# Performance work log

Measured on AMD Instinct MI355X. Metric: run time of the kernel, lower is better.

The kernel has to match this reference:

```python
import jax, jax.numpy as jnp
import numpy as np

SESSION_CHANNELS = [128, 160, 192, 224, 240, 248, 252, 256]  # per-session channel counts
N_SESS = len(SESSION_CHANNELS)
B, MAX_C, MAX_T = 16, 256, 4096
HID, N_SRC = 512, 256


def setup_inputs() -> dict:
    key = jax.random.key(0)
    ks = jax.random.split(key, 7)
    session_ids = jax.random.randint(ks[0], (B,), 0, N_SESS)
    chan_table = jnp.asarray(SESSION_CHANNELS)
    channel_counts = chan_table[session_ids]
    seq_lens = jax.random.randint(ks[1], (B,), MAX_T // 2, MAX_T + 1)
    x = jax.random.normal(ks[2], (B, MAX_C, MAX_T), jnp.float32)
    # zero-pad beyond true channels and true time (as the docstring states)
    cmask = (jnp.arange(MAX_C)[None, :] < channel_counts[:, None]).astype(x.dtype)
    tmask = (jnp.arange(MAX_T)[None, :] < seq_lens[:, None]).astype(x.dtype)
    x = x * cmask[:, :, None] * tmask[:, None, :]
    # per-session Linear(num_channels -> HID), padded to MAX_C rows (torch-style uniform init)
    lim1 = 1.0 / np.sqrt(MAX_C)
    W_sess = jax.random.uniform(ks[3], (N_SESS, MAX_C, HID), jnp.float32, -lim1, lim1)
    b_sess = jax.random.uniform(ks[4], (N_SESS, HID), jnp.float32, -lim1, lim1)
    lim2 = 1.0 / np.sqrt(HID)
    W2 = jax.random.uniform(ks[5], (HID, N_SRC), jnp.float32, -lim2, lim2)
    b2 = jax.random.uniform(ks[6], (N_SRC,), jnp.float32, -lim2, lim2)
    return dict(x=x, session_ids=session_ids, channel_counts=channel_counts,
                seq_lens=seq_lens, W_sess=W_sess, b_sess=b_sess, W2=W2, b2=b2)


def reference(x, session_ids, channel_counts, seq_lens, W_sess, b_sess, W2, b2):
    # mask padded channels so the full-width contraction equals the sliced per-sample matmul
    cmask = (jnp.arange(x.shape[1])[None, :] < channel_counts[:, None]).astype(x.dtype)
    xm = x * cmask[:, :, None]                       # (B, Max_C, Max_T)
    W = W_sess[session_ids]                          # (B, Max_C, HID) gathered per sample
    b = b_sess[session_ids]                          # (B, HID)
    h = jnp.einsum('bct,bch->bht', xm, W) + b[:, :, None]
    h = jax.nn.gelu(h, approximate=False)            # torch nn.GELU default is exact erf
    out = jnp.einsum('bht,hs->bst', h, W2) + b2[None, :, None]  # (B, N_SRC, Max_T)
    tmask = (jnp.arange(x.shape[2])[None, :] < seq_lens[:, None]).astype(x.dtype)
    return out * tmask[:, None, :]
```

## Files before the change

### kernel.cpp

```cpp
#include <hip/hip_runtime.h>

typedef __attribute__((ext_vector_type(8))) _Float16 f16x8;
typedef __attribute__((ext_vector_type(4))) _Float16 f16x4;
typedef __attribute__((ext_vector_type(4))) float f32x4;

#define NB 16
#define MAXC 256
#define MAXT 4096
#define HID 512
#define NSRC 256
#define TT 64

__device__ __forceinline__ float gelu_fast(float x) {
  float p = x * x;
  float q = __builtin_fmaf(p, -0.10294336f, -2.30220778f);
  float e = __builtin_amdgcn_exp2f(x * q);
  return x * __builtin_amdgcn_rcpf(1.0f + e);
}

__global__ void transpose_cvt_kernel(const float* __restrict__ src,
                                     _Float16* __restrict__ dst, int R, int C) {
  __shared__ float tile[32][33];
  const float* s = src + (size_t)blockIdx.z * R * C;
  _Float16* d = dst + (size_t)blockIdx.z * R * C;
  int c0 = blockIdx.x * 32, r0 = blockIdx.y * 32;
  int tx = threadIdx.x, ty = threadIdx.y;
  for (int i = ty; i < 32; i += 8)
    tile[i][tx] = s[(size_t)(r0 + i) * C + (c0 + tx)];
  __syncthreads();
  for (int i = ty; i < 32; i += 8)
    d[(size_t)(c0 + i) * R + (r0 + tx)] = (_Float16)tile[tx][i];
}

__global__ __launch_bounds__(512, 4)
void fused_sess_proj_kernel(const float* __restrict__ x,
                            const int* __restrict__ sess_ids,
                            const int* __restrict__ seq_lens,
                            const _Float16* __restrict__ W1t,
                            const float* __restrict__ b_sess,
                            const _Float16* __restrict__ W2t,
                            const float* __restrict__ b2,
                            float* __restrict__ out) {
  int wg = blockIdx.x;
  int b = wg >> 6;
  int t0 = (wg & 63) * TT;
  int seqlen = seq_lens[b];
  int tid = threadIdx.x;

  if (t0 >= seqlen) {
    int row = tid >> 1;
    int part = tid & 1;
    float* po = out + ((size_t)b * NSRC + row) * MAXT + t0 + part * 32;
    f32x4 z = {0.f, 0.f, 0.f, 0.f};
    #pragma unroll
    for (int i = 0; i < 8; ++i) *(f32x4*)(po + i * 4) = z;
    return;
  }

  __shared__ _Float16 Xs[TT * MAXC];
  __shared__ _Float16 Hs[TT * 256];

  {
    int c = tid & 255;
    int th = tid >> 8;
    const float* xp = x + ((size_t)b * MAXC + c) * MAXT + t0 + th * 32;
    #pragma unroll
    for (int i = 0; i < 8; ++i) {
      f32x4 v = *(const f32x4*)(xp + i * 4);
      #pragma unroll
      for (int k = 0; k < 4; ++k) {
        int t = th * 32 + i * 4 + k;
        Xs[t * 256 + (c ^ ((t & 7) << 3))] = (_Float16)v[k];
      }
    }
  }
  __syncthreads();

  int lane = tid & 63;
  int w = tid >> 6;
  int lg = lane >> 4;
  int lr = lane & 15;
  int sid = sess_ids[b];
  const _Float16* W1s = W1t + (size_t)sid * HID * MAXC;

  f32x4 acc2[2][4];
  #pragma unroll
  for (int mi = 0; mi < 2; ++mi) {
    f32x4 bv = *(const f32x4*)(b2 + w * 32 + mi * 16 + lg * 4);
    #pragma unroll
    for (int ni = 0; ni < 4; ++ni) acc2[mi][ni] = bv;
  }

  #pragma unroll
  for (int ch = 0; ch < 2; ++ch) {
    f32x4 acc1[2][4];
    #pragma unroll
    for (int mi = 0; mi < 2; ++mi) {
      f32x4 bv = *(const f32x4*)(b_sess + sid * HID + ch * 256 + w * 32 + mi * 16 + lg * 4);
      #pragma unroll
      for (int ni = 0; ni < 4; ++ni) acc1[mi][ni] = bv;
    }
    #pragma unroll
    for (int ks = 0; ks < 8; ++ks) {
      int k0 = ks * 32;
      f16x8 af[2], bf[4];
      #pragma unroll
      for (int mi = 0; mi < 2; ++mi)
        af[mi] = *(const f16x8*)(W1s +
            (size_t)(ch * 256 + w * 32 + mi * 16 + lr) * MAXC + k0 + lg * 8);
      #pragma unroll
      for (int ni = 0; ni < 4; ++ni) {
        int t = ni * 16 + lr;
        bf[ni] = *(const f16x8*)(&Xs[t * 256 + ((k0 + lg * 8) ^ ((t & 7) << 3))]);
      }
      #pragma unroll
      for (int mi = 0; mi < 2; ++mi)
        #pragma unroll
        for (int ni = 0; ni < 4; ++ni)
          acc1[mi][ni] = __builtin_amdgcn_mfma_f32_16x16x32_f16(af[mi], bf[ni], acc1[mi][ni], 0, 0, 0);
    }
    #pragma unroll
    for (int mi = 0; mi < 2; ++mi) {
      int hh = w * 32 + mi * 16 + lg * 4;
      #pragma unroll
      for (int ni = 0; ni < 4; ++ni) {
        int t = ni * 16 + lr;
        f16x4 g;
        #pragma unroll
        for (int r = 0; r < 4; ++r) g[r] = (_Float16)gelu_fast(acc1[mi][ni][r]);
        *(f16x4*)(&Hs[t * 256 + (hh ^ ((t & 7) << 3))]) = g;
      }
    }
    __syncthreads();
    #pragma unroll
    for (int ks = 0; ks < 8; ++ks) {
      int k0 = ks * 32;
      f16x8 af[2], bf[4];
      #pragma unroll
      for (int mi = 0; mi < 2; ++mi)
        af[mi] = *(const f16x8*)(W2t +
            (size_t)(w * 32 + mi * 16 + lr) * HID + ch * 256 + k0 + lg * 8);
      #pragma unroll
      for (int ni = 0; ni < 4; ++ni) {
        int t = ni * 16 + lr;
        bf[ni] = *(const f16x8*)(&Hs[t * 256 + ((k0 + lg * 8) ^ ((t & 7) << 3))]);
      }
      #pragma unroll
      for (int mi = 0; mi < 2; ++mi)
        #pragma unroll
        for (int ni = 0; ni < 4; ++ni)
          acc2[mi][ni] = __builtin_amdgcn_mfma_f32_16x16x32_f16(af[mi], bf[ni], acc2[mi][ni], 0, 0, 0);
    }
    __syncthreads();
  }

  #pragma unroll
  for (int mi = 0; mi < 2; ++mi) {
    int s0 = w * 32 + mi * 16 + lg * 4;
    #pragma unroll
    for (int ni = 0; ni < 4; ++ni) {
      int t = t0 + ni * 16 + lr;
      float m = (t < seqlen) ? 1.0f : 0.0f;
      #pragma unroll
      for (int r = 0; r < 4; ++r)
        out[((size_t)b * NSRC + s0 + r) * MAXT + t] = acc2[mi][ni][r] * m;
    }
  }
}

extern "C" void kernel_launch(void* const* d_in, const int* in_sizes, int n_in,
                              void* d_out, int out_size, void* d_ws, size_t ws_size,
                              hipStream_t stream) {
  const float* x      = (const float*)d_in[0];
  const int* sess     = (const int*)d_in[1];
  const int* seq      = (const int*)d_in[3];
  const float* W_sess = (const float*)d_in[4];
  const float* b_sess = (const float*)d_in[5];
  const float* W2     = (const float*)d_in[6];
  const float* b2     = (const float*)d_in[7];
  float* out = (float*)d_out;

  _Float16* W1t = (_Float16*)d_ws;
  _Float16* W2t = (_Float16*)((char*)d_ws + (size_t)8 * HID * MAXC * sizeof(_Float16));

  dim3 tb(32, 8);
  transpose_cvt_kernel<<<dim3(HID / 32, MAXC / 32, 8), tb, 0, stream>>>(W_sess, W1t, MAXC, HID);
  transpose_cvt_kernel<<<dim3(NSRC / 32, HID / 32, 1), tb, 0, stream>>>(W2, W2t, HID, NSRC);

  fused_sess_proj_kernel<<<dim3(NB * (MAXT / TT)), dim3(512), 0, stream>>>(
      x, sess, seq, W1t, b_sess, W2t, b2, out);
}
```

Before: 90.30 us.

## Retile fused MLP to 32-token blocks with 32x32x16 MFMA and 4 waves

Halves the time tile to 32 tokens and uses 256-thread blocks with 32x32x16 MFMA instructions, giving each wave a 64-row slice of the output. The X load now packs two channels per convert and store, the swizzle widens to 32 rows, and the barriers switch to a lighter lgkmcnt-only form, with the trailing barrier on the last chunk removed. MFMA issue is wrapped in setprio. The smaller tile doubles the block count and cuts LDS per block, which should raise occupancy and skip padded tokens more finely, at the cost of reading the weights from global memory twice as often per token.

```diff
diff --git a/kernel.cpp b/kernel.cpp
--- a/kernel.cpp
+++ b/kernel.cpp
@@ -2,14 +2,24 @@
 
 typedef __attribute__((ext_vector_type(8))) _Float16 f16x8;
 typedef __attribute__((ext_vector_type(4))) _Float16 f16x4;
+typedef __attribute__((ext_vector_type(2))) __fp16 fp16v2;
 typedef __attribute__((ext_vector_type(4))) float f32x4;
+typedef __attribute__((ext_vector_type(16))) float f32x16;
 
 #define NB 16
 #define MAXC 256
 #define MAXT 4096
 #define HID 512
 #define NSRC 256
-#define TT 64
+#define TT 32
+
+#define BAR() asm volatile("s_waitcnt lgkmcnt(0)\n\ts_barrier" ::: "memory")
+
+#define MFMA32(a, b, c) __builtin_amdgcn_mfma_f32_32x32x16_f16(a, b, c, 0, 0, 0)
+
+__device__ __forceinline__ int swz(int t, int col) {
+  return t * 256 + (col ^ ((t & 31) << 3));
+}
 
 __device__ __forceinline__ float gelu_fast(float x) {
   float p = x * x;
@@ -32,7 +42,7 @@
     d[(size_t)(c0 + i) * R + (r0 + tx)] = (_Float16)tile[tx][i];
 }
 
-__global__ __launch_bounds__(512, 4)
+__global__ __launch_bounds__(256, 4)
 void fused_sess_proj_kernel(const float* __restrict__ x,
                             const int* __restrict__ sess_ids,
                             const int* __restrict__ seq_lens,
@@ -42,15 +52,13 @@
                             const float* __restrict__ b2,
                             float* __restrict__ out) {
   int wg = blockIdx.x;
-  int b = wg >> 6;
-  int t0 = (wg & 63) * TT;
+  int b = wg >> 7;
+  int t0 = (wg & 127) * TT;
   int seqlen = seq_lens[b];
   int tid = threadIdx.x;
 
   if (t0 >= seqlen) {
-    int row = tid >> 1;
-    int part = tid & 1;
-    float* po = out + ((size_t)b * NSRC + row) * MAXT + t0 + part * 32;
+    float* po = out + ((size_t)b * NSRC + tid) * MAXT + t0;
     f32x4 z = {0.f, 0.f, 0.f, 0.f};
     #pragma unroll
     for (int i = 0; i < 8; ++i) *(f32x4*)(po + i * 4) = z;
@@ -60,112 +68,110 @@
   __shared__ _Float16 Xs[TT * MAXC];
   __shared__ _Float16 Hs[TT * 256];
 
+  int lane = tid & 63;
+  int w = tid >> 6;
+  int lm = lane & 31;
+  int kl = lane >> 5;
+  int sid = sess_ids[b];
+  const _Float16* W1s = W1t + (size_t)sid * HID * MAXC;
+
   {
-    int c = tid & 255;
-    int th = tid >> 8;
-    const float* xp = x + ((size_t)b * MAXC + c) * MAXT + t0 + th * 32;
+    int c2 = (tid & 127) * 2;
+    int th = tid >> 7;
+    const float* xp = x + ((size_t)b * MAXC + c2) * MAXT + t0 + th * 16;
     #pragma unroll
-    for (int i = 0; i < 8; ++i) {
-      f32x4 v = *(const f32x4*)(xp + i * 4);
+    for (int half = 0; half < 2; ++half) {
+      f32x4 va[2], vb[2];
       #pragma unroll
-      for (int k = 0; k < 4; ++k) {
-        int t = th * 32 + i * 4 + k;
-        Xs[t * 256 + (c ^ ((t & 7) << 3))] = (_Float16)v[k];
+      for (int i = 0; i < 2; ++i) va[i] = *(const f32x4*)(xp + half * 8 + i * 4);
+      #pragma unroll
+      for (int i = 0; i < 2; ++i) vb[i] = *(const f32x4*)(xp + MAXT + half * 8 + i * 4);
+      #pragma unroll
+      for (int k = 0; k < 8; ++k) {
+        int t = th * 16 + half * 8 + k;
+        fp16v2 p = __builtin_amdgcn_cvt_pkrtz(va[k >> 2][k & 3], vb[k >> 2][k & 3]);
+        *(fp16v2*)(&Xs[swz(t, c2)]) = p;
       }
     }
   }
-  __syncthreads();
+  BAR();
 
-  int lane = tid & 63;
-  int w = tid >> 6;
-  int lg = lane >> 4;
-  int lr = lane & 15;
-  int sid = sess_ids[b];
-  const _Float16* W1s = W1t + (size_t)sid * HID * MAXC;
-
-  f32x4 acc2[2][4];
-  #pragma unroll
-  for (int mi = 0; mi < 2; ++mi) {
-    f32x4 bv = *(const f32x4*)(b2 + w * 32 + mi * 16 + lg * 4);
-    #pragma unroll
-    for (int ni = 0; ni < 4; ++ni) acc2[mi][ni] = bv;
-  }
+  f32x16 acc2[2];
 
   #pragma unroll
   for (int ch = 0; ch < 2; ++ch) {
-    f32x4 acc1[2][4];
+    int chb = ch * 256;
+
+    f32x16 acc1[2];
     #pragma unroll
-    for (int mi = 0; mi < 2; ++mi) {
-      f32x4 bv = *(const f32x4*)(b_sess + sid * HID + ch * 256 + w * 32 + mi * 16 + lg * 4);
+    for (int mi = 0; mi < 2; ++mi)
       #pragma unroll
-      for (int ni = 0; ni < 4; ++ni) acc1[mi][ni] = bv;
+      for (int q = 0; q < 4; ++q) {
+        f32x4 bv = *(const f32x4*)(b_sess + sid * HID + chb + w * 64 + mi * 32 + q * 8 + kl * 4);
+        #pragma unroll
+        for (int r = 0; r < 4; ++r) acc1[mi][q * 4 + r] = bv[r];
+      }
+
+    const _Float16* w1p = W1s + (size_t)(chb + w * 64 + lm) * MAXC + kl * 8;
+    #pragma unroll
+    for (int ks = 0; ks < 16; ++ks) {
+      f16x8 af0 = *(const f16x8*)(w1p + ks * 16);
+      f16x8 af1 = *(const f16x8*)(w1p + 32 * MAXC + ks * 16);
+      f16x8 bf = *(const f16x8*)(&Xs[swz(lm, ks * 16 + kl * 8)]);
+      __builtin_amdgcn_s_setprio(1);
+      acc1[0] = MFMA32(af0, bf, acc1[0]);
+      acc1[1] = MFMA32(af1, bf, acc1[1]);
+      __builtin_amdgcn_s_setprio(0);
     }
+
     #pragma unroll
-    for (int ks = 0; ks < 8; ++ks) {
-      int k0 = ks * 32;
-      f16x8 af[2], bf[4];
+    for (int mi = 0; mi < 2; ++mi)
       #pragma unroll
-      for (int mi = 0; mi < 2; ++mi)
-        af[mi] = *(const f16x8*)(W1s +
-            (size_t)(ch * 256 + w * 32 + mi * 16 + lr) * MAXC + k0 + lg * 8);
-      #pragma unroll
-      for (int ni = 0; ni < 4; ++ni) {
-        int t = ni * 16 + lr;
-        bf[ni] = *(const f16x8*)(&Xs[t * 256 + ((k0 + lg * 8) ^ ((t & 7) << 3))]);
+      for (int q = 0; q < 4; ++q) {
+        int hh = w * 64 + mi * 32 + q * 8 + kl * 4;
+        f16x4 g;
+        #pragma unroll
+        for (int r = 0; r < 4; ++r) g[r] = (_Float16)gelu_fast(acc1[mi][q * 4 + r]);
+        *(f16x4*)(&Hs[swz(lm, hh)]) = g;
       }
+
+    if (ch == 0) {
       #pragma unroll
       for (int mi = 0; mi < 2; ++mi)
         #pragma unroll
-        for (int ni = 0; ni < 4; ++ni)
-          acc1[mi][ni] = __builtin_amdgcn_mfma_f32_16x16x32_f16(af[mi], bf[ni], acc1[mi][ni], 0, 0, 0);
+        for (int q = 0; q < 4; ++q) {
+          f32x4 bv = *(const f32x4*)(b2 + w * 64 + mi * 32 + q * 8 + kl * 4);
+          #pragma unroll
+          for (int r = 0; r < 4; ++r) acc2[mi][q * 4 + r] = bv[r];
+        }
     }
+    BAR();
+
+    const _Float16* w2p = W2t + (size_t)(w * 64 + lm) * HID + chb + kl * 8;
     #pragma unroll
-    for (int mi = 0; mi < 2; ++mi) {
-      int hh = w * 32 + mi * 16 + lg * 4;
-      #pragma unroll
-      for (int ni = 0; ni < 4; ++ni) {
-        int t = ni * 16 + lr;
-        f16x4 g;
-        #pragma unroll
-        for (int r = 0; r < 4; ++r) g[r] = (_Float16)gelu_fast(acc1[mi][ni][r]);
-        *(f16x4*)(&Hs[t * 256 + (hh ^ ((t & 7) << 3))]) = g;
-      }
+    for (int ks = 0; ks < 16; ++ks) {
+      f16x8 af0 = *(const f16x8*)(w2p + ks * 16);
+      f16x8 af1 = *(const f16x8*)(w2p + 32 * HID + ks * 16);
+      f16x8 bf = *(const f16x8*)(&Hs[swz(lm, ks * 16 + kl * 8)]);
+      __builtin_amdgcn_s_setprio(1);
+      acc2[0] = MFMA32(af0, bf, acc2[0]);
+      acc2[1] = MFMA32(af1, bf, acc2[1]);
+      __builtin_amdgcn_s_setprio(0);
     }
-    __syncthreads();
-    #pragma unroll
-    for (int ks = 0; ks < 8; ++ks) {
-      int k0 = ks * 32;
-      f16x8 af[2], bf[4];
-      #pragma unroll
-      for (int mi = 0; mi < 2; ++mi)
-        af[mi] = *(const f16x8*)(W2t +
-            (size_t)(w * 32 + mi * 16 + lr) * HID + ch * 256 + k0 + lg * 8);
-      #pragma unroll
-      for (int ni = 0; ni < 4; ++ni) {
-        int t = ni * 16 + lr;
-        bf[ni] = *(const f16x8*)(&Hs[t * 256 + ((k0 + lg * 8) ^ ((t & 7) << 3))]);
-      }
-      #pragma unroll
-      for (int mi = 0; mi < 2; ++mi)
-        #pragma unroll
-        for (int ni = 0; ni < 4; ++ni)
-          acc2[mi][ni] = __builtin_amdgcn_mfma_f32_16x16x32_f16(af[mi], bf[ni], acc2[mi][ni], 0, 0, 0);
-    }
-    __syncthreads();
+    if (ch == 0) BAR();
   }
 
+  int t = t0 + lm;
+  float m = (t < seqlen) ? 1.0f : 0.0f;
   #pragma unroll
-  for (int mi = 0; mi < 2; ++mi) {
-    int s0 = w * 32 + mi * 16 + lg * 4;
+  for (int mi = 0; mi < 2; ++mi)
     #pragma unroll
-    for (int ni = 0; ni < 4; ++ni) {
-      int t = t0 + ni * 16 + lr;
-      float m = (t < seqlen) ? 1.0f : 0.0f;
+    for (int q = 0; q < 4; ++q) {
+      int s0 = w * 64 + mi * 32 + q * 8 + kl * 4;
       #pragma unroll
       for (int r = 0; r < 4; ++r)
-        out[((size_t)b * NSRC + s0 + r) * MAXT + t] = acc2[mi][ni][r] * m;
+        out[((size_t)b * NSRC + s0 + r) * MAXT + t] = acc2[mi][q * 4 + r] * m;
     }
-  }
 }
 
 extern "C" void kernel_launch(void* const* d_in, const int* in_sizes, int n_in,
@@ -187,6 +193,6 @@
   transpose_cvt_kernel<<<dim3(HID / 32, MAXC / 32, 8), tb, 0, stream>>>(W_sess, W1t, MAXC, HID);
   transpose_cvt_kernel<<<dim3(NSRC / 32, HID / 32, 1), tb, 0, stream>>>(W2, W2t, HID, NSRC);
 
-  fused_sess_proj_kernel<<<dim3(NB * (MAXT / TT)), dim3(512), 0, stream>>>(
+  fused_sess_proj_kernel<<<dim3(NB * (MAXT / TT)), dim3(256), 0, stream>>>(
       x, sess, seq, W1t, b_sess, W2t, b2, out);
 }
```

Measured after the change: 150.3 us. 66.4% more time.

## Split fused projection into two tiled GEMM kernels with fp16 hidden buffer

Applied to the files above, without the earlier changes.

Replaces the single fused kernel, which kept the whole hidden activation in LDS per 64-step time tile, with two separate GEMM kernels using 128x128 tiles, K-chunked LDS staging and 4x4 MFMA tiles per wave. The GELU hidden activation is written to a global fp16 workspace buffer (B x T x HID) and read back by the second GEMM. The goal is higher MFMA register reuse and better occupancy, and it also adds pkrtz conversion and setprio around the MFMA blocks. The cost is an extra global round trip for the hidden tensor, about 64MB written and then read, plus one more launch.

```diff
diff --git a/kernel.cpp b/kernel.cpp
--- a/kernel.cpp
+++ b/kernel.cpp
@@ -2,6 +2,7 @@
 
 typedef __attribute__((ext_vector_type(8))) _Float16 f16x8;
 typedef __attribute__((ext_vector_type(4))) _Float16 f16x4;
+typedef __attribute__((ext_vector_type(2))) __fp16 fp16v2;
 typedef __attribute__((ext_vector_type(4))) float f32x4;
 
 #define NB 16
@@ -9,7 +10,10 @@
 #define MAXT 4096
 #define HID 512
 #define NSRC 256
-#define TT 64
+
+#define BAR() asm volatile("s_waitcnt lgkmcnt(0)\n\ts_barrier" ::: "memory")
+
+#define MFMA(a, b, c) __builtin_amdgcn_mfma_f32_16x16x32_f16(a, b, c, 0, 0, 0)
 
 __device__ __forceinline__ float gelu_fast(float x) {
   float p = x * x;
@@ -32,138 +36,198 @@
     d[(size_t)(c0 + i) * R + (r0 + tx)] = (_Float16)tile[tx][i];
 }
 
-__global__ __launch_bounds__(512, 4)
-void fused_sess_proj_kernel(const float* __restrict__ x,
-                            const int* __restrict__ sess_ids,
-                            const int* __restrict__ seq_lens,
-                            const _Float16* __restrict__ W1t,
-                            const float* __restrict__ b_sess,
-                            const _Float16* __restrict__ W2t,
-                            const float* __restrict__ b2,
-                            float* __restrict__ out) {
+
+__global__ __launch_bounds__(256, 3)
+void gemm1_kernel(const float* __restrict__ x,
+                  const int* __restrict__ sess_ids,
+                  const int* __restrict__ seq_lens,
+                  const _Float16* __restrict__ W1t,
+                  const float* __restrict__ b_sess,
+                  _Float16* __restrict__ h_t) {
   int wg = blockIdx.x;
+  int nt = wg & 31;
+  int mt = (wg >> 5) & 3;
+  int b = wg >> 7;
+  int tb0 = nt * 128, h0 = mt * 128;
+  int seqlen = seq_lens[b];
+  if (tb0 >= seqlen) return;
+  int sid = sess_ids[b];
+  const _Float16* W = W1t + (size_t)sid * HID * MAXC + (size_t)h0 * MAXC;
+
+  __shared__ _Float16 As[128 * 64];
+  __shared__ _Float16 Bs[128 * 64];
+
+  int tid = threadIdx.x;
+  int lane = tid & 63, w = tid >> 6;
+  int wr = w >> 1, wc = w & 1;
+  int lg = lane >> 4, lr = lane & 15;
+
+  f32x4 acc[4][4];
+  #pragma unroll
+  for (int mi = 0; mi < 4; ++mi) {
+    f32x4 bv = *(const f32x4*)(b_sess + sid * HID + h0 + wr * 64 + mi * 16 + lg * 4);
+    #pragma unroll
+    for (int ni = 0; ni < 4; ++ni) acc[mi][ni] = bv;
+  }
+
+  int ar = tid >> 1, ah = tid & 1;
+  int c2 = (tid & 31) * 2, ts = tid >> 5;
+
+  #pragma unroll 1
+  for (int kc = 0; kc < 4; ++kc) {
+    int c0 = kc * 64;
+    {
+      const _Float16* ga = W + (size_t)ar * MAXC + c0 + ah * 32;
+      #pragma unroll
+      for (int j = 0; j < 4; ++j) {
+        f16x8 v = *(const f16x8*)(ga + j * 8);
+        *(f16x8*)(&As[ar * 64 + (((ah * 4 + j) ^ (ar & 7)) * 8)]) = v;
+      }
+    }
+    {
+      const float* gx = x + ((size_t)b * MAXC + c0 + c2) * MAXT + tb0 + ts * 16;
+      f32x4 va[4], vb[4];
+      #pragma unroll
+      for (int j = 0; j < 4; ++j) va[j] = *(const f32x4*)(gx + j * 4);
+      #pragma unroll
+      for (int j = 0; j < 4; ++j) vb[j] = *(const f32x4*)(gx + MAXT + j * 4);
+      #pragma unroll
+      for (int k = 0; k < 16; ++k) {
+        int t = ts * 16 + k;
+        fp16v2 p = __builtin_amdgcn_cvt_pkrtz(va[k >> 2][k & 3], vb[k >> 2][k & 3]);
+        *(fp16v2*)(&Bs[t * 64 + (((c2 >> 3) ^ (t & 7)) * 8) + (c2 & 7)]) = p;
+      }
+    }
+    BAR();
+    #pragma unroll
+    for (int slot = 0; slot < 2; ++slot) {
+      f16x8 af[4], bf[4];
+      #pragma unroll
+      for (int mi = 0; mi < 4; ++mi) {
+        int row = wr * 64 + mi * 16 + lr;
+        af[mi] = *(const f16x8*)(&As[row * 64 + (((slot * 4 + lg) ^ (row & 7)) * 8)]);
+      }
+      #pragma unroll
+      for (int ni = 0; ni < 4; ++ni) {
+        int t = wc * 64 + ni * 16 + lr;
+        bf[ni] = *(const f16x8*)(&Bs[t * 64 + (((slot * 4 + lg) ^ (t & 7)) * 8)]);
+      }
+      __builtin_amdgcn_s_setprio(1);
+      #pragma unroll
+      for (int mi = 0; mi < 4; ++mi)
+        #pragma unroll
+        for (int ni = 0; ni < 4; ++ni)
+          acc[mi][ni] = MFMA(af[mi], bf[ni], acc[mi][ni]);
+      __builtin_amdgcn_s_setprio(0);
+    }
+    BAR();
+  }
+
+  _Float16* hp = h_t + (size_t)b * MAXT * HID;
+  #pragma unroll
+  for (int mi = 0; mi < 4; ++mi) {
+    int h = h0 + wr * 64 + mi * 16 + lg * 4;
+    #pragma unroll
+    for (int ni = 0; ni < 4; ++ni) {
+      int t = tb0 + wc * 64 + ni * 16 + lr;
+      f16x4 g;
+      #pragma unroll
+      for (int r = 0; r < 4; ++r) g[r] = (_Float16)gelu_fast(acc[mi][ni][r]);
+      *(f16x4*)(hp + (size_t)t * HID + h) = g;
+    }
+  }
+}
+
+__global__ __launch_bounds__(256, 4)
+void gemm2_kernel(const int* __restrict__ seq_lens,
+                  const _Float16* __restrict__ W2t,
+                  const float* __restrict__ b2,
+                  const _Float16* __restrict__ h_t,
+                  float* __restrict__ out) {
+  int wg = blockIdx.x;
+  int nt = wg & 31;
+  int mt = (wg >> 5) & 1;
   int b = wg >> 6;
-  int t0 = (wg & 63) * TT;
+  int tb0 = nt * 128, s0 = mt * 128;
   int seqlen = seq_lens[b];
   int tid = threadIdx.x;
 
-  if (t0 >= seqlen) {
-    int row = tid >> 1;
-    int part = tid & 1;
-    float* po = out + ((size_t)b * NSRC + row) * MAXT + t0 + part * 32;
+  if (tb0 >= seqlen) {
+    int sr = tid >> 1, tq = (tid & 1) * 64;
+    float* po = out + ((size_t)b * NSRC + s0 + sr) * MAXT + tb0 + tq;
     f32x4 z = {0.f, 0.f, 0.f, 0.f};
     #pragma unroll
-    for (int i = 0; i < 8; ++i) *(f32x4*)(po + i * 4) = z;
+    for (int i = 0; i < 16; ++i) *(f32x4*)(po + i * 4) = z;
     return;
   }
 
-  __shared__ _Float16 Xs[TT * MAXC];
-  __shared__ _Float16 Hs[TT * 256];
-
-  {
-    int c = tid & 255;
-    int th = tid >> 8;
-    const float* xp = x + ((size_t)b * MAXC + c) * MAXT + t0 + th * 32;
-    #pragma unroll
-    for (int i = 0; i < 8; ++i) {
-      f32x4 v = *(const f32x4*)(xp + i * 4);
-      #pragma unroll
-      for (int k = 0; k < 4; ++k) {
-        int t = th * 32 + i * 4 + k;
-        Xs[t * 256 + (c ^ ((t & 7) << 3))] = (_Float16)v[k];
-      }
-    }
-  }
-  __syncthreads();
-
-  int lane = tid & 63;
-  int w = tid >> 6;
-  int lg = lane >> 4;
-  int lr = lane & 15;
-  int sid = sess_ids[b];
-  const _Float16* W1s = W1t + (size_t)sid * HID * MAXC;
-
-  f32x4 acc2[2][4];
-  #pragma unroll
-  for (int mi = 0; mi < 2; ++mi) {
-    f32x4 bv = *(const f32x4*)(b2 + w * 32 + mi * 16 + lg * 4);
-    #pragma unroll
-    for (int ni = 0; ni < 4; ++ni) acc2[mi][ni] = bv;
-  }
-
-  #pragma unroll
-  for (int ch = 0; ch < 2; ++ch) {
-    f32x4 acc1[2][4];
-    #pragma unroll
-    for (int mi = 0; mi < 2; ++mi) {
-      f32x4 bv = *(const f32x4*)(b_sess + sid * HID + ch * 256 + w * 32 + mi * 16 + lg * 4);
-      #pragma unroll
-      for (int ni = 0; ni < 4; ++ni) acc1[mi][ni] = bv;
-    }
-    #pragma unroll
-    for (int ks = 0; ks < 8; ++ks) {
-      int k0 = ks * 32;
-      f16x8 af[2], bf[4];
-      #pragma unroll
-      for (int mi = 0; mi < 2; ++mi)
-        af[mi] = *(const f16x8*)(W1s +
-            (size_t)(ch * 256 + w * 32 + mi * 16 + lr) * MAXC + k0 + lg * 8);
+  __shared__ _Float16 As[128 * 64];
+  __shared__ _Float16 Bs[128 * 64];
+
+  int lane = tid & 63, w = tid >> 6;
+  int wr = w >> 1, wc = w & 1;
+  int lg = lane >> 4, lr = lane & 15;
+
+  f32x4 acc[4][4];
+  #pragma unroll
+  for (int mi = 0; mi < 4; ++mi) {
+    f32x4 bv = *(const f32x4*)(b2 + s0 + wr * 64 + mi * 16 + lg * 4);
+    #pragma unroll
+    for (int ni = 0; ni < 4; ++ni) acc[mi][ni] = bv;
+  }
+
+  int ar = tid >> 1, ah = tid & 1;
+  const _Float16* WA = W2t + (size_t)(s0 + ar) * HID + ah * 32;
+  const _Float16* HB = h_t + ((size_t)b * MAXT + tb0 + ar) * HID + ah * 32;
+
+  #pragma unroll 1
+  for (int kc = 0; kc < 8; ++kc) {
+    int k0 = kc * 64;
+    #pragma unroll
+    for (int j = 0; j < 4; ++j) {
+      f16x8 v = *(const f16x8*)(WA + k0 + j * 8);
+      *(f16x8*)(&As[ar * 64 + (((ah * 4 + j) ^ (ar & 7)) * 8)]) = v;
+    }
+    #pragma unroll
+    for (int j = 0; j < 4; ++j) {
+      f16x8 v = *(const f16x8*)(HB + k0 + j * 8);
+      *(f16x8*)(&Bs[ar * 64 + (((ah * 4 + j) ^ (ar & 7)) * 8)]) = v;
+    }
+    BAR();
+    #pragma unroll
+    for (int slot = 0; slot < 2; ++slot) {
+      f16x8 af[4], bf[4];
+      #pragma unroll
+      for (int mi = 0; mi < 4; ++mi) {
+        int row = wr * 64 + mi * 16 + lr;
+        af[mi] = *(const f16x8*)(&As[row * 64 + (((slot * 4 + lg) ^ (row & 7)) * 8)]);
+      }
       #pragma unroll
       for (int ni = 0; ni < 4; ++ni) {
-        int t = ni * 16 + lr;
-        bf[ni] = *(const f16x8*)(&Xs[t * 256 + ((k0 + lg * 8) ^ ((t & 7) << 3))]);
-      }
-      #pragma unroll
-      for (int mi = 0; mi < 2; ++mi)
+        int t = wc * 64 + ni * 16 + lr;
+        bf[ni] = *(const f16x8*)(&Bs[t * 64 + (((slot * 4 + lg) ^ (t & 7)) * 8)]);
+      }
+      __builtin_amdgcn_s_setprio(1);
+      #pragma unroll
+      for (int mi = 0; mi < 4; ++mi)
         #pragma unroll
         for (int ni = 0; ni < 4; ++ni)
-          acc1[mi][ni] = __builtin_amdgcn_mfma_f32_16x16x32_f16(af[mi], bf[ni], acc1[mi][ni], 0, 0, 0);
-    }
-    #pragma unroll
-    for (int mi = 0; mi < 2; ++mi) {
-      int hh = w * 32 + mi * 16 + lg * 4;
-      #pragma unroll
-      for (int ni = 0; ni < 4; ++ni) {
-        int t = ni * 16 + lr;
-        f16x4 g;
-        #pragma unroll
-        for (int r = 0; r < 4; ++r) g[r] = (_Float16)gelu_fast(acc1[mi][ni][r]);
-        *(f16x4*)(&Hs[t * 256 + (hh ^ ((t & 7) << 3))]) = g;
-      }
-    }
-    __syncthreads();
-    #pragma unroll
-    for (int ks = 0; ks < 8; ++ks) {
-      int k0 = ks * 32;
-      f16x8 af[2], bf[4];
-      #pragma unroll
-      for (int mi = 0; mi < 2; ++mi)
-        af[mi] = *(const f16x8*)(W2t +
-            (size_t)(w * 32 + mi * 16 + lr) * HID + ch * 256 + k0 + lg * 8);
-      #pragma unroll
-      for (int ni = 0; ni < 4; ++ni) {
-        int t = ni * 16 + lr;
-        bf[ni] = *(const f16x8*)(&Hs[t * 256 + ((k0 + lg * 8) ^ ((t & 7) << 3))]);
-      }
-      #pragma unroll
-      for (int mi = 0; mi < 2; ++mi)
-        #pragma unroll
-        for (int ni = 0; ni < 4; ++ni)
-          acc2[mi][ni] = __builtin_amdgcn_mfma_f32_16x16x32_f16(af[mi], bf[ni], acc2[mi][ni], 0, 0, 0);
-    }
-    __syncthreads();
-  }
-
-  #pragma unroll
-  for (int mi = 0; mi < 2; ++mi) {
-    int s0 = w * 32 + mi * 16 + lg * 4;
+          acc[mi][ni] = MFMA(af[mi], bf[ni], acc[mi][ni]);
+      __builtin_amdgcn_s_setprio(0);
+    }
+    BAR();
+  }
+
+  #pragma unroll
+  for (int mi = 0; mi < 4; ++mi) {
+    int s = s0 + wr * 64 + mi * 16 + lg * 4;
     #pragma unroll
     for (int ni = 0; ni < 4; ++ni) {
-      int t = t0 + ni * 16 + lr;
+      int t = tb0 + wc * 64 + ni * 16 + lr;
       float m = (t < seqlen) ? 1.0f : 0.0f;
       #pragma unroll
       for (int r = 0; r < 4; ++r)
-        out[((size_t)b * NSRC + s0 + r) * MAXT + t] = acc2[mi][ni][r] * m;
+        out[((size_t)b * NSRC + s + r) * MAXT + t] = acc[mi][ni][r] * m;
     }
   }
 }
@@ -181,12 +245,13 @@
   float* out = (float*)d_out;
 
   _Float16* W1t = (_Float16*)d_ws;
-  _Float16* W2t = (_Float16*)((char*)d_ws + (size_t)8 * HID * MAXC * sizeof(_Float16));
+  _Float16* W2t = (_Float16*)((char*)d_ws + (size_t)2 * 1024 * 1024);
+  _Float16* h_t = (_Float16*)((char*)d_ws + (size_t)2 * 1024 * 1024 + 256 * 1024);
 
   dim3 tb(32, 8);
   transpose_cvt_kernel<<<dim3(HID / 32, MAXC / 32, 8), tb, 0, stream>>>(W_sess, W1t, MAXC, HID);
   transpose_cvt_kernel<<<dim3(NSRC / 32, HID / 32, 1), tb, 0, stream>>>(W2, W2t, HID, NSRC);
 
-  fused_sess_proj_kernel<<<dim3(NB * (MAXT / TT)), dim3(512), 0, stream>>>(
-      x, sess, seq, W1t, b_sess, W2t, b2, out);
-}
+  gemm1_kernel<<<dim3(NB * 4 * 32), dim3(256), 0, stream>>>(x, sess, seq, W1t, b_sess, h_t);
+  gemm2_kernel<<<dim3(NB * 2 * 32), dim3(256), 0, stream>>>(seq, W2t, b2, h_t, out);
+}
```

Result: slower. 96.37 us (+6.7%).
